# Optimization experiments

Hardware: AMD Instinct MI355X
Metric: run time of the kernel (lower is better)

Reference implementation:

```python
import jax, jax.numpy as jnp
import numpy as np

B, S, DIM, SDIM = 4, 4096, 1024, 256


def setup_inputs() -> dict:
    key = jax.random.key(0)
    ks = jax.random.split(key, 10)
    def lin(k, din, dout):
        return jax.random.normal(k, (din, dout), jnp.float32) / np.float32(np.sqrt(din))
    return {
        "x": jax.random.normal(ks[0], (B, S, DIM), jnp.float32),
        "ln_g": jnp.ones((DIM,), jnp.float32),
        "ln_b": jnp.zeros((DIM,), jnp.float32),
        "mix_w": jax.random.normal(ks[1], (DIM, 1, 3), jnp.float32) * 0.3,  # depthwise conv kernel
        "mix_b": jnp.zeros((DIM,), jnp.float32),
        "Wi": lin(ks[2], DIM, DIM), "bi": jnp.zeros((DIM,), jnp.float32),
        "Wsin": lin(ks[3], DIM, SDIM), "bsin": jnp.zeros((SDIM,), jnp.float32),
        "Wd": lin(ks[4], DIM, SDIM), "bd": jnp.zeros((SDIM,), jnp.float32),
        "Wsel": lin(ks[5], DIM, SDIM), "bsel": jnp.zeros((SDIM,), jnp.float32),
        "Wso": lin(ks[6], SDIM, DIM), "bso": jnp.zeros((DIM,), jnp.float32),
        "Wg": lin(ks[7], DIM, DIM), "bg": jnp.zeros((DIM,), jnp.float32),
        "Wout": lin(ks[8], DIM, DIM), "bout": jnp.zeros((DIM,), jnp.float32),
    }


def reference(x, ln_g, ln_b, mix_w, mix_b, Wi, bi, Wsin, bsin, Wd, bd,
              Wsel, bsel, Wso, bso, Wg, bg, Wout, bout):
    eps = 1e-5
    # LayerNorm over last dim
    mu = jnp.mean(x, axis=-1, keepdims=True)
    var = jnp.mean(jnp.square(x - mu), axis=-1, keepdims=True)
    h = (x - mu) * jax.lax.rsqrt(var + eps) * ln_g + ln_b
    # depthwise Conv1d, kernel=3, padding=1, groups=dim
    hc = jnp.transpose(h, (0, 2, 1))  # [B, C, L]
    mixed = jax.lax.conv_general_dilated(
        hc, mix_w, window_strides=(1,), padding=[(1, 1)],
        dimension_numbers=("NCH", "OIH", "NCH"), feature_group_count=hc.shape[1])
    mixed = jnp.transpose(mixed + mix_b[None, :, None], (0, 2, 1))  # [B, S, D]
    u = jnp.tanh(mixed @ Wi + bi)                 # [B, S, D]
    x_state = jnp.tanh(mixed @ Wsin + bsin)       # [B, S, N]
    decay = jax.nn.sigmoid(mixed @ Wd + bd)       # [B, S, N]
    select = jax.nn.sigmoid(mixed @ Wsel + bsel)  # [B, S, N]
    # sequential linear recurrence: state = d*state + (1-d)*x_state
    def step(state, inp):
        dt, xt = inp
        state = dt * state + (1.0 - dt) * xt
        return state, state
    init = jnp.zeros((x.shape[0], x_state.shape[-1]), x.dtype)
    _, states = jax.lax.scan(step, init,
                             (jnp.swapaxes(decay, 0, 1), jnp.swapaxes(x_state, 0, 1)))
    states = jnp.swapaxes(states, 0, 1)           # [B, S, N]
    y = (select * states) @ Wso + bso             # [B, S, D]
    g = jax.nn.sigmoid(mixed @ Wg + bg)
    out = (g * y + (1.0 - g) * u) @ Wout + bout
    return x + out
```

## Files before the change

kernel.cpp:

```cpp
#include <hip/hip_runtime.h>
#include <hip/hip_bf16.h>
#include <math.h>

typedef __bf16 bf16_t;
typedef __bf16 bf16x8 __attribute__((ext_vector_type(8)));
typedef __bf16 bf16x4 __attribute__((ext_vector_type(4)));
typedef float  f32x4  __attribute__((ext_vector_type(4)));

#define B_ 4
#define S_ 4096
#define D_ 1024
#define N_ 256
#define M_ (B_*S_)

__device__ __forceinline__ float fsig(float x){
    return __builtin_amdgcn_rcpf(1.0f + __expf(-x));
}
__device__ __forceinline__ float ftanh(float x){
    return 1.0f - 2.0f*__builtin_amdgcn_rcpf(1.0f + __expf(2.0f*x));
}

__device__ __forceinline__ void gload_lds16(const void* g, void* l){
    __builtin_amdgcn_global_load_lds(
        (const __attribute__((address_space(1))) unsigned int*)g,
        (__attribute__((address_space(3))) unsigned int*)l, 16, 0, 0);
}

struct TJobs {
    const float* in[7];
    bf16_t*      out[7];
    int R[7];
    int C[7];
};

__global__ void transpose_all(TJobs j){
    int z = blockIdx.z;
    int R = j.R[z], C = j.C[z];
    int c0 = blockIdx.x*32, r0 = blockIdx.y*32;
    if (c0 >= C || r0 >= R) return;
    __shared__ float tile[32][33];
    int tx = threadIdx.x, ty = threadIdx.y;
    const float* in = j.in[z];
    bf16_t* out = j.out[z];
    #pragma unroll
    for (int i=0;i<32;i+=8)
        tile[ty+i][tx] = in[(size_t)(r0+ty+i)*C + (c0+tx)];
    __syncthreads();
    #pragma unroll
    for (int i=0;i<32;i+=8)
        out[(size_t)(c0+ty+i)*R + (r0+tx)] = (bf16_t)tile[tx][ty+i];
}

__global__ void ln_kernel(const float* __restrict__ x, const float* __restrict__ gw,
                          const float* __restrict__ bw, bf16_t* __restrict__ h){
    int row = blockIdx.x;
    int t = threadIdx.x;
    float4 v = ((const float4*)(x + (size_t)row*D_))[t];
    float s = v.x+v.y+v.z+v.w;
    float q = v.x*v.x+v.y*v.y+v.z*v.z+v.w*v.w;
    #pragma unroll
    for (int o=1;o<64;o<<=1){ s += __shfl_xor(s,o,64); q += __shfl_xor(q,o,64); }
    __shared__ float sw[4], sq[4];
    int wid = t>>6;
    if ((t&63)==0){ sw[wid]=s; sq[wid]=q; }
    __syncthreads();
    s = sw[0]+sw[1]+sw[2]+sw[3];
    q = sq[0]+sq[1]+sq[2]+sq[3];
    float mu = s*(1.0f/D_);
    float rs = rsqrtf(q*(1.0f/D_) - mu*mu + 1e-5f);
    float4 gv = ((const float4*)gw)[t];
    float4 bv = ((const float4*)bw)[t];
    bf16x4 o4;
    o4[0] = (bf16_t)((v.x-mu)*rs*gv.x + bv.x);
    o4[1] = (bf16_t)((v.y-mu)*rs*gv.y + bv.y);
    o4[2] = (bf16_t)((v.z-mu)*rs*gv.z + bv.z);
    o4[3] = (bf16_t)((v.w-mu)*rs*gv.w + bv.w);
    *(bf16x4*)(h + (size_t)row*D_ + t*4) = o4;
}

__global__ void conv_kernel(const bf16_t* __restrict__ h, const float* __restrict__ w,
                            const float* __restrict__ mb, bf16_t* __restrict__ mix){
    int idx = blockIdx.x*256 + threadIdx.x;
    int g8  = idx & 127;
    int row = idx >> 7;
    int s   = row & (S_-1);
    int d0  = g8*8;
    const bf16_t* hr = h + (size_t)row*D_ + d0;
    bf16x8 cur = *(const bf16x8*)hr;
    bf16x8 prv, nxt;
    #pragma unroll
    for (int i=0;i<8;i++){ prv[i]=(bf16_t)0.0f; nxt[i]=(bf16_t)0.0f; }
    if (s > 0)      prv = *(const bf16x8*)(hr - D_);
    if (s < S_-1)   nxt = *(const bf16x8*)(hr + D_);
    bf16x8 ov;
    #pragma unroll
    for (int i=0;i<8;i++){
        int d = d0+i;
        float o = (float)prv[i]*w[d*3] + (float)cur[i]*w[d*3+1] + (float)nxt[i]*w[d*3+2] + mb[d];
        ov[i] = (bf16_t)o;
    }
    *(bf16x8*)(mix + (size_t)row*D_ + d0) = ov;
}

struct Epi {
    const float *b0,*b1,*b2,*b3,*b4;
    bf16_t *u, *g, *z;
    bf16_t *xs, *dc, *sel;
    const bf16_t *gbuf, *ubuf;
    const float *resid;
    float *outp;
};

#define WAITV3()  asm volatile("s_waitcnt vmcnt(3)" ::: "memory")
#define WAITV0()  asm volatile("s_waitcnt vmcnt(0)" ::: "memory")
#define WAITLGK0() asm volatile("s_waitcnt lgkmcnt(0)" ::: "memory")
#define CFENCE()  asm volatile("" ::: "memory")
#define BARR()    __builtin_amdgcn_s_barrier()

template<int MODE>
__global__ __launch_bounds__(512,4)
void gemm128(const bf16_t* __restrict__ A, const bf16_t* __restrict__ Bt,
             int K, Epi e){
    extern __shared__ __align__(16) char lds[];
    const int ATILE = 8192;
    const int BTILE = 16384;
    int t = threadIdx.x;
    int wave = t>>6, lane = t&63;
    int wm = (wave>>2)*64;
    int wn = (wave&3)*64;
    int lm = lane&15, quad = lane>>4;

    int flat = blockIdx.y*gridDim.x + blockIdx.x;
    int nwg  = gridDim.x*gridDim.y;
    int wg   = (flat&7)*(nwg>>3) + (flat>>3);
    int m0 = (wg & 127)*128;
    int n0 = (wg >> 7)*256;
    int NT = K>>5;

    const bf16_t* gA = A  + (size_t)(m0 + (t>>2))*K + (t&3)*8;
    const bf16_t* gB = Bt + (size_t)(n0 + (t>>2))*K + (t&3)*8;

    auto stage = [&](int kt, int buf){
        const bf16_t* a = gA + kt*32;
        const bf16_t* b = gB + kt*32;
        char* da = lds + buf*ATILE + t*16;
        char* db = lds + 16384 + buf*BTILE + t*16;
        gload_lds16(a, da);
        gload_lds16(b, db);
        gload_lds16(b + (size_t)128*K, db + 8192);
    };

    int raBase = (wm+lm)*64 + quad*16;
    int rbBase = (wn+lm)*64 + quad*16;

    f32x4 acc[4][4];
    #pragma unroll
    for (int i=0;i<4;i++)
        #pragma unroll
        for (int j=0;j<4;j++)
            #pragma unroll
            for (int r=0;r<4;r++) acc[i][j][r]=0.0f;

    bf16x8 aF[4], bF[4];

    stage(0,0);
    stage(1,1);
    WAITV3();
    BARR();
    CFENCE();

    for (int kt=0; kt<NT; ++kt){
        int buf = kt&1;
        const char* pa = lds + buf*ATILE + raBase;
        const char* pb = lds + 16384 + buf*BTILE + rbBase;

        #pragma unroll
        for (int j=0;j<4;j++) bF[j] = *(const bf16x8*)(pb + j*1024);
        #pragma unroll
        for (int i=0;i<4;i++) aF[i] = *(const bf16x8*)(pa + i*1024);

        #pragma unroll
        for (int i=0;i<4;i++)
            #pragma unroll
            for (int j=0;j<4;j++)
                acc[i][j] = __builtin_amdgcn_mfma_f32_16x16x32_bf16(aF[i], bF[j], acc[i][j], 0,0,0);

        WAITLGK0();
        BARR();
        CFENCE();
        if (kt+2 < NT){
            stage(kt+2, buf);
            WAITV3();
            BARR();
            CFENCE();
        } else if (kt+1 < NT){
            WAITV0();
            BARR();
            CFENCE();
        }
    }
    __syncthreads();

    if (MODE==0 || MODE==1){
        const float* bp = e.b0; int cbase = 0; bf16_t* dst = 0; int width = D_;
        bool ut = true;
        if (MODE==0){
            ut = (n0 < 1280);
            if (n0 < 1024){ bp=e.b0; cbase=n0; dst=e.u; width=D_; }
            else if (n0 < 1792){
                int sub=(n0-1024)>>8;
                bp  = sub==0? e.b1 : sub==1? e.b2 : e.b3;
                dst = sub==0? e.xs : sub==1? e.dc : e.sel;
                cbase = 0; width = N_;
            } else { bp=e.b4; cbase=n0-1792; dst=e.g; width=D_; }
        } else {
            bp = e.b0; cbase = n0; width = D_;
        }
        bf16_t* Tb = (bf16_t*)lds;
        #pragma unroll
        for (int h=0; h<2; h++){
            if (h) __syncthreads();
            if (wm == h*64){
                #pragma unroll
                for (int ii=0;ii<4;ii++){
                    #pragma unroll
                    for (int j=0;j<4;j++){
                        float bv = bp[(MODE==0?cbase:n0) + wn + j*16 + lm];
                        #pragma unroll
                        for (int r=0;r<4;r++){
                            float v = acc[ii][j][r] + bv;
                            if (MODE==0) v = ut ? ftanh(v) : fsig(v);
                            Tb[(ii*16+quad*4+r)*264 + wn + j*16 + lm] = (bf16_t)v;
                        }
                    }
                }
            }
            __syncthreads();
            if (MODE==0){
                #pragma unroll
                for (int it=0; it<4; it++){
                    int idx = it*512 + t;
                    int row = idx>>5, c8 = idx&31;
                    bf16x8 v = *(const bf16x8*)&Tb[row*264 + c8*8];
                    *(bf16x8*)&dst[(size_t)(m0 + h*64 + row)*width + cbase + c8*8] = v;
                }
            } else {
                #pragma unroll
                for (int it=0; it<4; it++){
                    int idx = it*512 + t;
                    int row = idx>>5, c8 = idx&31;
                    bf16x8 y = *(const bf16x8*)&Tb[row*264 + c8*8];
                    size_t gi = (size_t)(m0 + h*64 + row)*D_ + n0 + c8*8;
                    bf16x8 gv = *(const bf16x8*)&e.gbuf[gi];
                    bf16x8 uv = *(const bf16x8*)&e.ubuf[gi];
                    bf16x8 o;
                    #pragma unroll
                    for (int q=0;q<8;q++){
                        float gf = (float)gv[q];
                        o[q] = (bf16_t)(gf*(float)y[q] + (1.0f-gf)*(float)uv[q]);
                    }
                    *(bf16x8*)&e.z[gi] = o;
                }
            }
        }
    } else {
        float* T = (float*)lds;
        #pragma unroll
        for (int pZ=0; pZ<4; pZ++){
            if (pZ) __syncthreads();
            if (wm == (pZ>>1)*64){
                int ib = (pZ&1)*2;
                #pragma unroll
                for (int ii=0;ii<2;ii++){
                    #pragma unroll
                    for (int j=0;j<4;j++)
                        #pragma unroll
                        for (int r=0;r<4;r++)
                            T[(ii*16+quad*4+r)*260 + wn + j*16 + lm] = acc[ib+ii][j][r];
                }
            }
            __syncthreads();
            #pragma unroll
            for (int it=0; it<4; it++){
                int idx = it*512 + t;
                int row = idx>>6, c4 = idx&63;
                f32x4 v = *(const f32x4*)&T[row*260 + c4*4];
                size_t gi = (size_t)(m0 + pZ*32 + row)*D_ + n0 + c4*4;
                float4 res = *(const float4*)&e.resid[gi];
                float4 bb  = *(const float4*)&e.b0[n0 + c4*4];
                float4 o;
                o.x = v[0]+res.x+bb.x; o.y = v[1]+res.y+bb.y;
                o.z = v[2]+res.z+bb.z; o.w = v[3]+res.w+bb.w;
                *(float4*)&e.outp[gi] = o;
            }
        }
    }
}

__global__ void scan_p1(const bf16_t* __restrict__ dc, const bf16_t* __restrict__ xs,
                        float* __restrict__ aggA, float* __restrict__ aggB){
    int bc = blockIdx.x;
    int b = bc>>6, ch = bc&63;
    int n = threadIdx.x;
    size_t base = ((size_t)b*S_ + ch*64)*N_ + n;
    float A = 1.0f, Bc = 0.0f;
    for (int t=0;t<64;t++){
        float d = (float)dc[base + (size_t)t*N_];
        float x = (float)xs[base + (size_t)t*N_];
        A  = d*A;
        Bc = d*Bc + (1.0f-d)*x;
    }
    aggA[(size_t)bc*N_+n]=A; aggB[(size_t)bc*N_+n]=Bc;
}

__global__ void scan_p2(const float* __restrict__ aggA, const float* __restrict__ aggB,
                        float* __restrict__ pre){
    int b = blockIdx.x, n = threadIdx.x;
    float s = 0.0f;
    for (int ch=0; ch<64; ch++){
        size_t i = ((size_t)b*64+ch)*N_+n;
        pre[i] = s;
        s = aggA[i]*s + aggB[i];
    }
}

__global__ void scan_p3(const bf16_t* __restrict__ dc, const bf16_t* __restrict__ xs,
                        const bf16_t* __restrict__ sel, const float* __restrict__ pre,
                        bf16_t* __restrict__ ss){
    int bc = blockIdx.x;
    int b = bc>>6, ch = bc&63;
    int n = threadIdx.x;
    size_t base = ((size_t)b*S_ + ch*64)*N_ + n;
    float s = pre[(size_t)bc*N_+n];
    for (int t=0;t<64;t++){
        size_t i = base + (size_t)t*N_;
        float d = (float)dc[i], x = (float)xs[i];
        s = d*s + (1.0f-d)*x;
        ss[i] = (bf16_t)((float)sel[i]*s);
    }
}

extern "C" void kernel_launch(void* const* d_in, const int* in_sizes, int n_in,
                              void* d_out, int out_size, void* d_ws, size_t ws_size,
                              hipStream_t stream){
    const float* x    = (const float*)d_in[0];
    const float* ln_g = (const float*)d_in[1];
    const float* ln_b = (const float*)d_in[2];
    const float* mixw = (const float*)d_in[3];
    const float* mixb = (const float*)d_in[4];
    const float* Wi   = (const float*)d_in[5];
    const float* bi   = (const float*)d_in[6];
    const float* Wsin = (const float*)d_in[7];
    const float* bsin = (const float*)d_in[8];
    const float* Wd   = (const float*)d_in[9];
    const float* bd   = (const float*)d_in[10];
    const float* Wsel = (const float*)d_in[11];
    const float* bsel = (const float*)d_in[12];
    const float* Wso  = (const float*)d_in[13];
    const float* bso  = (const float*)d_in[14];
    const float* Wg   = (const float*)d_in[15];
    const float* bg   = (const float*)d_in[16];
    const float* Wout = (const float*)d_in[17];
    const float* bout = (const float*)d_in[18];
    float* out = (float*)d_out;

    char* p = (char*)d_ws;
    auto alloc = [&](size_t bytes)->char*{ char* r=p; p += (bytes+255)&~(size_t)255; return r; };
    bf16_t* hB    = (bf16_t*)alloc((size_t)M_*D_*2);
    bf16_t* mixB  = (bf16_t*)alloc((size_t)M_*D_*2);
    bf16_t* uB    = (bf16_t*)alloc((size_t)M_*D_*2);
    bf16_t* gB    = (bf16_t*)alloc((size_t)M_*D_*2);
    bf16_t* ssB   = (bf16_t*)alloc((size_t)M_*N_*2);
    bf16_t* xs    = (bf16_t*)alloc((size_t)M_*N_*2);
    bf16_t* dc    = (bf16_t*)alloc((size_t)M_*N_*2);
    bf16_t* sel   = (bf16_t*)alloc((size_t)M_*N_*2);
    bf16_t* WbigT = (bf16_t*)alloc((size_t)2816*1024*2);
    bf16_t* WsoT  = (bf16_t*)alloc(1024*256*2);
    bf16_t* WoutT = (bf16_t*)alloc(1024*1024*2);
    float*  aggA  = (float*)alloc((size_t)4*64*256*4);
    float*  aggB  = (float*)alloc((size_t)4*64*256*4);
    float*  pre   = (float*)alloc((size_t)4*64*256*4);
    bf16_t* zB = mixB;

    TJobs tj;
    tj.in[0]=Wi;   tj.out[0]=WbigT;            tj.R[0]=1024; tj.C[0]=1024;
    tj.in[1]=Wsin; tj.out[1]=WbigT+1024*1024;  tj.R[1]=1024; tj.C[1]=256;
    tj.in[2]=Wd;   tj.out[2]=WbigT+1280*1024;  tj.R[2]=1024; tj.C[2]=256;
    tj.in[3]=Wsel; tj.out[3]=WbigT+1536*1024;  tj.R[3]=1024; tj.C[3]=256;
    tj.in[4]=Wg;   tj.out[4]=WbigT+(size_t)1792*1024; tj.R[4]=1024; tj.C[4]=1024;
    tj.in[5]=Wso;  tj.out[5]=WsoT;             tj.R[5]=256;  tj.C[5]=1024;
    tj.in[6]=Wout; tj.out[6]=WoutT;            tj.R[6]=1024; tj.C[6]=1024;
    transpose_all<<<dim3(32,32,7), dim3(32,8), 0, stream>>>(tj);

    ln_kernel  <<<M_, 256, 0, stream>>>(x, ln_g, ln_b, hB);
    conv_kernel<<<M_*128/256, 256, 0, stream>>>(hB, mixw, mixb, mixB);

    Epi e0 = {};
    e0.b0=bi; e0.b1=bsin; e0.b2=bd; e0.b3=bsel; e0.b4=bg;
    e0.u=uB; e0.g=gB; e0.xs=xs; e0.dc=dc; e0.sel=sel;
    gemm128<0><<<dim3(M_/128, 11), 512, 49152, stream>>>(mixB, WbigT, 1024, e0);

    scan_p1<<<4*64, 256, 0, stream>>>(dc, xs, aggA, aggB);
    scan_p2<<<4,    256, 0, stream>>>(aggA, aggB, pre);
    scan_p3<<<4*64, 256, 0, stream>>>(dc, xs, sel, pre, ssB);

    Epi e1 = {};
    e1.b0=bso; e1.gbuf=gB; e1.ubuf=uB; e1.z=zB;
    gemm128<1><<<dim3(M_/128, 4), 512, 49152, stream>>>(ssB, WsoT, 256, e1);

    Epi e2 = {};
    e2.b0=bout; e2.resid=x; e2.outp=out;
    gemm128<2><<<dim3(M_/128, 4), 512, 49152, stream>>>(zB, WoutT, 1024, e2);
}
```

Measured before the change: 404.7 us.

## Vectorize scan kernels, drop GEMM block swizzle, change LDS staging pitch

The chunked scan kernels now give each thread four channels using bf16x4 loads and float4 stores, so each block covers four chunks and the grid shrinks from 256 to 64 blocks. The GEMM drops the XCD-aware workgroup remap in favour of direct blockIdx tiling. The bf16 epilogue staging pitch changes from 264 to 260 elements, which alters the LDS bank pattern. Wider loads cut instruction count in the scans, but only 64 blocks leave most CUs idle, and losing the swizzle may reduce L2 reuse across chiplets.

```diff
diff --git a/kernel.cpp b/kernel.cpp
--- a/kernel.cpp
+++ b/kernel.cpp
@@ -130,11 +130,8 @@
     int wn = (wave&3)*64;
     int lm = lane&15, quad = lane>>4;
 
-    int flat = blockIdx.y*gridDim.x + blockIdx.x;
-    int nwg  = gridDim.x*gridDim.y;
-    int wg   = (flat&7)*(nwg>>3) + (flat>>3);
-    int m0 = (wg & 127)*128;
-    int n0 = (wg >> 7)*256;
+    int m0 = blockIdx.x*128;
+    int n0 = blockIdx.y*256;
     int NT = K>>5;
 
     const bf16_t* gA = A  + (size_t)(m0 + (t>>2))*K + (t&3)*8;
@@ -230,7 +227,7 @@
                         for (int r=0;r<4;r++){
                             float v = acc[ii][j][r] + bv;
                             if (MODE==0) v = ut ? ftanh(v) : fsig(v);
-                            Tb[(ii*16+quad*4+r)*264 + wn + j*16 + lm] = (bf16_t)v;
+                            Tb[(ii*16+quad*4+r)*260 + wn + j*16 + lm] = (bf16_t)v;
                         }
                     }
                 }
@@ -241,7 +238,7 @@
                 for (int it=0; it<4; it++){
                     int idx = it*512 + t;
                     int row = idx>>5, c8 = idx&31;
-                    bf16x8 v = *(const bf16x8*)&Tb[row*264 + c8*8];
+                    bf16x8 v = *(const bf16x8*)&Tb[row*260 + c8*8];
                     *(bf16x8*)&dst[(size_t)(m0 + h*64 + row)*width + cbase + c8*8] = v;
                 }
             } else {
@@ -249,7 +246,7 @@
                 for (int it=0; it<4; it++){
                     int idx = it*512 + t;
                     int row = idx>>5, c8 = idx&31;
-                    bf16x8 y = *(const bf16x8*)&Tb[row*264 + c8*8];
+                    bf16x8 y = *(const bf16x8*)&Tb[row*260 + c8*8];
                     size_t gi = (size_t)(m0 + h*64 + row)*D_ + n0 + c8*8;
                     bf16x8 gv = *(const bf16x8*)&e.gbuf[gi];
                     bf16x8 uv = *(const bf16x8*)&e.ubuf[gi];
@@ -299,18 +296,25 @@
 
 __global__ void scan_p1(const bf16_t* __restrict__ dc, const bf16_t* __restrict__ xs,
                         float* __restrict__ aggA, float* __restrict__ aggB){
-    int bc = blockIdx.x;
-    int b = bc>>6, ch = bc&63;
-    int n = threadIdx.x;
-    size_t base = ((size_t)b*S_ + ch*64)*N_ + n;
-    float A = 1.0f, Bc = 0.0f;
+    int wg4 = blockIdx.x*4 + (threadIdx.x>>6);
+    int b = wg4>>6, ch = wg4&63;
+    int l4 = (threadIdx.x&63)*4;
+    size_t base = ((size_t)b*S_ + ch*64)*N_ + l4;
+    float A0=1.f,A1=1.f,A2=1.f,A3=1.f, B0=0.f,B1=0.f,B2=0.f,B3=0.f;
     for (int t=0;t<64;t++){
-        float d = (float)dc[base + (size_t)t*N_];
-        float x = (float)xs[base + (size_t)t*N_];
-        A  = d*A;
-        Bc = d*Bc + (1.0f-d)*x;
-    }
-    aggA[(size_t)bc*N_+n]=A; aggB[(size_t)bc*N_+n]=Bc;
+        bf16x4 d4 = *(const bf16x4*)(dc + base + (size_t)t*N_);
+        bf16x4 x4 = *(const bf16x4*)(xs + base + (size_t)t*N_);
+        float d;
+        d=(float)d4[0]; A0*=d; B0=d*B0+(1.f-d)*(float)x4[0];
+        d=(float)d4[1]; A1*=d; B1=d*B1+(1.f-d)*(float)x4[1];
+        d=(float)d4[2]; A2*=d; B2=d*B2+(1.f-d)*(float)x4[2];
+        d=(float)d4[3]; A3*=d; B3=d*B3+(1.f-d)*(float)x4[3];
+    }
+    size_t o = (size_t)wg4*N_ + l4;
+    float4 av; av.x=A0; av.y=A1; av.z=A2; av.w=A3;
+    float4 bv; bv.x=B0; bv.y=B1; bv.z=B2; bv.w=B3;
+    *(float4*)(aggA+o) = av;
+    *(float4*)(aggB+o) = bv;
 }
 
 __global__ void scan_p2(const float* __restrict__ aggA, const float* __restrict__ aggB,
@@ -327,16 +331,29 @@
 __global__ void scan_p3(const bf16_t* __restrict__ dc, const bf16_t* __restrict__ xs,
                         const bf16_t* __restrict__ sel, const float* __restrict__ pre,
                         bf16_t* __restrict__ ss){
-    int bc = blockIdx.x;
-    int b = bc>>6, ch = bc&63;
-    int n = threadIdx.x;
-    size_t base = ((size_t)b*S_ + ch*64)*N_ + n;
-    float s = pre[(size_t)bc*N_+n];
+    int wg4 = blockIdx.x*4 + (threadIdx.x>>6);
+    int b = wg4>>6, ch = wg4&63;
+    int l4 = (threadIdx.x&63)*4;
+    size_t base = ((size_t)b*S_ + ch*64)*N_ + l4;
+    size_t o = (size_t)wg4*N_ + l4;
+    float4 pv = *(const float4*)(pre+o);
+    float s0=pv.x, s1=pv.y, s2=pv.z, s3=pv.w;
     for (int t=0;t<64;t++){
         size_t i = base + (size_t)t*N_;
-        float d = (float)dc[i], x = (float)xs[i];
-        s = d*s + (1.0f-d)*x;
-        ss[i] = (bf16_t)((float)sel[i]*s);
+        bf16x4 d4 = *(const bf16x4*)(dc+i);
+        bf16x4 x4 = *(const bf16x4*)(xs+i);
+        bf16x4 e4 = *(const bf16x4*)(sel+i);
+        float d;
+        d=(float)d4[0]; s0=d*s0+(1.f-d)*(float)x4[0];
+        d=(float)d4[1]; s1=d*s1+(1.f-d)*(float)x4[1];
+        d=(float)d4[2]; s2=d*s2+(1.f-d)*(float)x4[2];
+        d=(float)d4[3]; s3=d*s3+(1.f-d)*(float)x4[3];
+        bf16x4 o4;
+        o4[0]=(bf16_t)((float)e4[0]*s0);
+        o4[1]=(bf16_t)((float)e4[1]*s1);
+        o4[2]=(bf16_t)((float)e4[2]*s2);
+        o4[3]=(bf16_t)((float)e4[3]*s3);
+        *(bf16x4*)(ss+i) = o4;
     }
 }
 
@@ -400,9 +417,9 @@
     e0.u=uB; e0.g=gB; e0.xs=xs; e0.dc=dc; e0.sel=sel;
     gemm128<0><<<dim3(M_/128, 11), 512, 49152, stream>>>(mixB, WbigT, 1024, e0);
 
-    scan_p1<<<4*64, 256, 0, stream>>>(dc, xs, aggA, aggB);
-    scan_p2<<<4,    256, 0, stream>>>(aggA, aggB, pre);
-    scan_p3<<<4*64, 256, 0, stream>>>(dc, xs, sel, pre, ssB);
+    scan_p1<<<64, 256, 0, stream>>>(dc, xs, aggA, aggB);
+    scan_p2<<<4,  256, 0, stream>>>(aggA, aggB, pre);
+    scan_p3<<<64, 256, 0, stream>>>(dc, xs, sel, pre, ssB);
 
     Epi e1 = {};
     e1.b0=bso; e1.gbuf=gB; e1.ubuf=uB; e1.z=zB;
```

New measurement: 407.6 us. About the same (+0.7%).
